# Kernel optimization log

Hardware: AMD Instinct MI355X
Metric: run time of the kernel (lower is better)

## Reference

```python
import jax, jax.numpy as jnp
import numpy as np
import math

B, S, N_EMBD, HEAD_SIZE = 32, 2048, 64, 64

def setup_inputs() -> dict:
    key = jax.random.key(0)
    k1, k2, k3, k4 = jax.random.split(key, 4)
    inputs = jax.random.normal(k1, (B, S, N_EMBD), dtype=jnp.float32)
    # nn.Linear(n_embd, head_size, bias=False) weights: shape (head_size, n_embd)
    scale = 1.0 / math.sqrt(N_EMBD)
    Wq = jax.random.normal(k2, (HEAD_SIZE, N_EMBD), dtype=jnp.float32) * scale
    Wk = jax.random.normal(k3, (HEAD_SIZE, N_EMBD), dtype=jnp.float32) * scale
    Wv = jax.random.normal(k4, (HEAD_SIZE, N_EMBD), dtype=jnp.float32) * scale
    return {"inputs": inputs, "Wq": Wq, "Wk": Wk, "Wv": Wv}

def reference(inputs, Wq, Wk, Wv):
    # q, k, v: [B, S, head_size]
    q = jnp.einsum('bse,he->bsh', inputs, Wq)
    k = jnp.einsum('bse,he->bsh', inputs, Wk)
    v = jnp.einsum('bse,he->bsh', inputs, Wv)
    scores = jnp.einsum('bqh,bkh->bqk', q, k) / jnp.sqrt(jnp.float32(HEAD_SIZE))
    # NOTE: the original torch code calls scores.masked_fill(...) out-of-place
    # and discards the result, so NO causal mask is actually applied.
    attention = jax.nn.softmax(scores, axis=-1)
    out = jnp.einsum('bqk,bkh->bqh', attention, v)  # [B, S, head_size]
    return out
```

## Files before the change

### kernel.cpp

```cpp
#include <hip/hip_runtime.h>


#define BATCH 32
#define SEQ   2048
#define HS    64
#define QSCALE 0.18033688011112042f
#define OTS   72
#define MSTR  68

typedef _Float16 f16x8 __attribute__((ext_vector_type(8)));
typedef _Float16 f16x4 __attribute__((ext_vector_type(4)));
typedef float    f32x4 __attribute__((ext_vector_type(4)));
typedef unsigned int u32x4 __attribute__((ext_vector_type(4)));

__global__ __launch_bounds__(256) void proj_kernel(
    const float* __restrict__ x, const float* __restrict__ Wq,
    const float* __restrict__ Wk, const float* __restrict__ Wv,
    _Float16* __restrict__ Qh, _Float16* __restrict__ Kh,
    _Float16* __restrict__ Vt)
{
    __shared__ __align__(16) _Float16 Wl[3 * 4096];
    __shared__ __align__(16) _Float16 ot[64 * OTS];

    const int t    = threadIdx.x;
    const int w    = t >> 6;
    const int lane = t & 63;
    const int lo   = lane & 15;
    const int quad = lane >> 4;

    {
#pragma unroll
        for (int c = 0; c < 6; ++c) {
            int id  = c * 256 + t;
            int m   = id >> 9;
            int rem = id & 511;
            int row = rem >> 3;
            int q8  = rem & 7;
            const float* Ws = (m == 0) ? Wq : ((m == 1) ? Wk : Wv);
            const float* sp = Ws + row * 64 + q8 * 8;
            float4 a0 = *(const float4*)sp;
            float4 a1 = *(const float4*)(sp + 4);
            float sc = (m == 0) ? QSCALE : 1.0f;
            f16x8 h;
            h[0]=(_Float16)(a0.x*sc); h[1]=(_Float16)(a0.y*sc);
            h[2]=(_Float16)(a0.z*sc); h[3]=(_Float16)(a0.w*sc);
            h[4]=(_Float16)(a1.x*sc); h[5]=(_Float16)(a1.y*sc);
            h[6]=(_Float16)(a1.z*sc); h[7]=(_Float16)(a1.w*sc);
            *(f16x8*)(Wl + m * 4096 + row * 64 + ((q8 ^ (row & 7)) << 3)) = h;
        }
    }

    const long blk0 = (long)blockIdx.x * 64;
    const int  b    = (int)(blk0 / SEQ);
    const int  s0   = (int)(blk0 % SEQ);
    const long rw   = blk0 + w * 16;

    const float* xp = x + (rw + lo) * HS + quad * 8;
    float4 x0 = *(const float4*)xp;
    float4 x1 = *(const float4*)(xp + 4);
    float4 x2 = *(const float4*)(xp + 32);
    float4 x3 = *(const float4*)(xp + 36);
    f16x8 xb0, xb1;
    xb0[0]=(_Float16)x0.x; xb0[1]=(_Float16)x0.y; xb0[2]=(_Float16)x0.z; xb0[3]=(_Float16)x0.w;
    xb0[4]=(_Float16)x1.x; xb0[5]=(_Float16)x1.y; xb0[6]=(_Float16)x1.z; xb0[7]=(_Float16)x1.w;
    xb1[0]=(_Float16)x2.x; xb1[1]=(_Float16)x2.y; xb1[2]=(_Float16)x2.z; xb1[3]=(_Float16)x2.w;
    xb1[4]=(_Float16)x3.x; xb1[5]=(_Float16)x3.y; xb1[6]=(_Float16)x3.z; xb1[7]=(_Float16)x3.w;

    __syncthreads();

#pragma unroll
    for (int m = 0; m < 3; ++m) {
        const _Float16* Wm = Wl + m * 4096;
        f32x4 acc[4];
#pragma unroll
        for (int nt = 0; nt < 4; ++nt) { acc[nt][0]=0.f; acc[nt][1]=0.f; acc[nt][2]=0.f; acc[nt][3]=0.f; }
#pragma unroll
        for (int nt = 0; nt < 4; ++nt) {
            f16x8 wa0 = *(const f16x8*)(Wm + (nt * 16 + lo) * 64 + (((quad    ) ^ (lo & 7)) << 3));
            f16x8 wa1 = *(const f16x8*)(Wm + (nt * 16 + lo) * 64 + (((4 + quad) ^ (lo & 7)) << 3));
            acc[nt] = __builtin_amdgcn_mfma_f32_16x16x32_f16(wa0, xb0, acc[nt], 0, 0, 0);
            acc[nt] = __builtin_amdgcn_mfma_f32_16x16x32_f16(wa1, xb1, acc[nt], 0, 0, 0);
        }
        if (m < 2) {
            _Float16* dst = (m == 0) ? Qh : Kh;
#pragma unroll
            for (int nt = 0; nt < 4; ++nt) {
                f16x4 pk;
                pk[0]=(_Float16)acc[nt][0]; pk[1]=(_Float16)acc[nt][1];
                pk[2]=(_Float16)acc[nt][2]; pk[3]=(_Float16)acc[nt][3];
                *(f16x4*)(dst + (rw + lo) * HS + nt * 16 + quad * 4) = pk;
            }
        } else {
#pragma unroll
            for (int nt = 0; nt < 4; ++nt)
#pragma unroll
                for (int r = 0; r < 4; ++r)
                    ot[(nt * 16 + quad * 4 + r) * OTS + w * 16 + lo] = (_Float16)acc[nt][r];
            __syncthreads();
            const int row = t >> 2, c = t & 3;
            f16x8 r0 = *(const f16x8*)(ot + row * OTS + c * 16);
            f16x8 r1 = *(const f16x8*)(ot + row * OTS + c * 16 + 8);
            _Float16* vd = Vt + ((long)b * HS + row) * SEQ + s0 + c * 16;
            *(f16x8*)vd       = r0;
            *(f16x8*)(vd + 8) = r1;
        }
    }
}

__global__ __launch_bounds__(256, 2) void attn_kernel(
    const _Float16* __restrict__ Q, const _Float16* __restrict__ K,
    const _Float16* __restrict__ Vt, float* __restrict__ out)
{
    __shared__ __align__(16) char smem[65536];
    _Float16* KVb  = (_Float16*)smem;
    float*    obuf = (float*)smem;
    float*    lbuf = obuf + 128 * MSTR;

    const int t    = threadIdx.x;
    const int w    = t >> 6;
    const int lane = t & 63;
    const int lo   = lane & 15;
    const int quad = lane >> 4;
    const int sr   = t >> 2, sc = t & 3;
    const int xr   = lo & 7;

    const int bid = blockIdx.x;
    const int b   = (bid & 7) | ((bid >> 7) << 3);
    const int qt  = (bid >> 3) & 15;
    const int q0  = qt * 128;
    const int qh  = w >> 1;
    const int kh  = w & 1;

    const _Float16* Qb = Q + ((long)b * SEQ + q0 + qh * 64) * HS;
    f16x8 qf[4][2];
#pragma unroll
    for (int q2 = 0; q2 < 4; ++q2) {
        qf[q2][0] = *(const f16x8*)(Qb + (q2 * 16 + lo) * HS + quad * 8);
        qf[q2][1] = *(const f16x8*)(Qb + (q2 * 16 + lo) * HS + 32 + quad * 8);
    }

    const _Float16* Kb = K  + (long)b * SEQ * HS;
    const _Float16* Vb = Vt + (long)b * HS * SEQ;

    const int pr  = (sr & 32) | ((sr & 4) << 2) | ((sr & 24) >> 1) | (sr & 3);
    const int kw0 = pr * 64 + (((2 * sc    ) ^ (pr & 7)) << 3);
    const int kw1 = pr * 64 + (((2 * sc + 1) ^ (pr & 7)) << 3);
    const int vw0 = 4096 + sr * 64 + (((2 * sc    ) ^ (sr & 7)) << 3);
    const int vw1 = 4096 + sr * 64 + (((2 * sc + 1) ^ (sr & 7)) << 3);

    const int kr0 = (kh * 32      + lo) * 64;
    const int kr1 = (kh * 32 + 16 + lo) * 64;
    const int g0  = ((quad    ) ^ xr) << 3;
    const int g1  = ((4 + quad) ^ xr) << 3;
    int voff[4];
#pragma unroll
    for (int ht = 0; ht < 4; ++ht)
        voff[ht] = 4096 + (ht * 16 + lo) * 64 + (((kh * 4 + quad) ^ xr) << 3);

    f32x4 o[4][4], ol[4];
#pragma unroll
    for (int q2 = 0; q2 < 4; ++q2) {
        ol[q2][0]=0.f; ol[q2][1]=0.f; ol[q2][2]=0.f; ol[q2][3]=0.f;
#pragma unroll
        for (int ht = 0; ht < 4; ++ht) { o[q2][ht][0]=0.f; o[q2][ht][1]=0.f; o[q2][ht][2]=0.f; o[q2][ht][3]=0.f; }
    }
    f32x4 zz; zz[0]=0.f; zz[1]=0.f; zz[2]=0.f; zz[3]=0.f;
    f16x8 ones;
#pragma unroll
    for (int j = 0; j < 8; ++j) ones[j] = (_Float16)1.0f;

    const int phase = qt << 1;
    const int key0 = (phase & 31) << 6;
    f16x8 kfA0 = *(const f16x8*)(Kb + (long)(key0 + sr) * HS + sc * 16);
    f16x8 kfB0 = *(const f16x8*)(Kb + (long)(key0 + sr) * HS + sc * 16 + 8);
    f16x8 vfA0 = *(const f16x8*)(Vb + (long)sr * SEQ + key0 + sc * 16);
    f16x8 vfB0 = *(const f16x8*)(Vb + (long)sr * SEQ + key0 + sc * 16 + 8);
    f16x8 kfA1 = *(const f16x8*)(Kb + (long)(key0 + 64 + sr) * HS + sc * 16);
    f16x8 kfB1 = *(const f16x8*)(Kb + (long)(key0 + 64 + sr) * HS + sc * 16 + 8);
    f16x8 vfA1 = *(const f16x8*)(Vb + (long)sr * SEQ + key0 + 64 + sc * 16);
    f16x8 vfB1 = *(const f16x8*)(Vb + (long)sr * SEQ + key0 + 64 + sc * 16 + 8);

    for (int kt2 = 0; kt2 < 16; ++kt2) {
        _Float16* Bp = KVb + (kt2 & 1) * 16384;
        *(f16x8*)(Bp + kw0) = kfA0;
        *(f16x8*)(Bp + kw1) = kfB0;
        *(f16x8*)(Bp + vw0) = vfA0;
        *(f16x8*)(Bp + vw1) = vfB0;
        *(f16x8*)(Bp + 8192 + kw0) = kfA1;
        *(f16x8*)(Bp + 8192 + kw1) = kfB1;
        *(f16x8*)(Bp + 8192 + vw0) = vfA1;
        *(f16x8*)(Bp + 8192 + vw1) = vfB1;

        const int keyn = ((2 * kt2 + 2 + phase) & 31) << 6;
        kfA0 = *(const f16x8*)(Kb + (long)(keyn + sr) * HS + sc * 16);
        kfB0 = *(const f16x8*)(Kb + (long)(keyn + sr) * HS + sc * 16 + 8);
        vfA0 = *(const f16x8*)(Vb + (long)sr * SEQ + keyn + sc * 16);
        vfB0 = *(const f16x8*)(Vb + (long)sr * SEQ + keyn + sc * 16 + 8);
        kfA1 = *(const f16x8*)(Kb + (long)(keyn + 64 + sr) * HS + sc * 16);
        kfB1 = *(const f16x8*)(Kb + (long)(keyn + 64 + sr) * HS + sc * 16 + 8);
        vfA1 = *(const f16x8*)(Vb + (long)sr * SEQ + keyn + 64 + sc * 16);
        vfB1 = *(const f16x8*)(Vb + (long)sr * SEQ + keyn + 64 + sc * 16 + 8);

        __syncthreads();

#pragma unroll
        for (int sub = 0; sub < 2; ++sub) {
            _Float16* Ksp = Bp + sub * 8192;

            f16x8 ka00 = *(const f16x8*)(Ksp + kr0 + g0);
            f16x8 ka01 = *(const f16x8*)(Ksp + kr0 + g1);
            f16x8 ka10 = *(const f16x8*)(Ksp + kr1 + g0);
            f16x8 ka11 = *(const f16x8*)(Ksp + kr1 + g1);

            f16x8 vbf[4];
#pragma unroll
            for (int ht = 0; ht < 4; ++ht)
                vbf[ht] = *(const f16x8*)(Ksp + voff[ht]);

#pragma unroll
            for (int q2 = 0; q2 < 4; ++q2) {
                f32x4 s0, s1;
                s0 = __builtin_amdgcn_mfma_f32_16x16x32_f16(ka00, qf[q2][0], zz, 0, 0, 0);
                s0 = __builtin_amdgcn_mfma_f32_16x16x32_f16(ka01, qf[q2][1], s0, 0, 0, 0);
                s1 = __builtin_amdgcn_mfma_f32_16x16x32_f16(ka10, qf[q2][0], zz, 0, 0, 0);
                s1 = __builtin_amdgcn_mfma_f32_16x16x32_f16(ka11, qf[q2][1], s1, 0, 0, 0);

                u32x4 pw;
                pw[0] = __builtin_bit_cast(unsigned int,
                        __builtin_amdgcn_cvt_pkrtz(__builtin_amdgcn_exp2f(s0[0]),
                                                   __builtin_amdgcn_exp2f(s0[1])));
                pw[1] = __builtin_bit_cast(unsigned int,
                        __builtin_amdgcn_cvt_pkrtz(__builtin_amdgcn_exp2f(s0[2]),
                                                   __builtin_amdgcn_exp2f(s0[3])));
                pw[2] = __builtin_bit_cast(unsigned int,
                        __builtin_amdgcn_cvt_pkrtz(__builtin_amdgcn_exp2f(s1[0]),
                                                   __builtin_amdgcn_exp2f(s1[1])));
                pw[3] = __builtin_bit_cast(unsigned int,
                        __builtin_amdgcn_cvt_pkrtz(__builtin_amdgcn_exp2f(s1[2]),
                                                   __builtin_amdgcn_exp2f(s1[3])));
                f16x8 pa = __builtin_bit_cast(f16x8, pw);

                ol[q2] = __builtin_amdgcn_mfma_f32_16x16x32_f16(pa, ones, ol[q2], 0, 0, 0);
#pragma unroll
                for (int ht = 0; ht < 4; ++ht)
                    o[q2][ht] = __builtin_amdgcn_mfma_f32_16x16x32_f16(pa, vbf[ht], o[q2][ht], 0, 0, 0);
            }
        }
    }

    __syncthreads();
    if (kh == 0) {
#pragma unroll
        for (int q2 = 0; q2 < 4; ++q2) {
#pragma unroll
            for (int ht = 0; ht < 4; ++ht)
#pragma unroll
                for (int r = 0; r < 4; ++r)
                    obuf[(qh * 64 + q2 * 16 + quad * 4 + r) * MSTR + ht * 16 + lo] = o[q2][ht][r];
            if (lo == 0) {
#pragma unroll
                for (int r = 0; r < 4; ++r)
                    lbuf[qh * 64 + q2 * 16 + quad * 4 + r] = ol[q2][r];
            }
        }
    }
    __syncthreads();
    if (kh == 1) {
#pragma unroll
        for (int q2 = 0; q2 < 4; ++q2) {
            float linv[4];
#pragma unroll
            for (int r = 0; r < 4; ++r)
                linv[r] = 1.0f / (lbuf[qh * 64 + q2 * 16 + quad * 4 + r] + ol[q2][r]);
#pragma unroll
            for (int ht = 0; ht < 4; ++ht)
#pragma unroll
                for (int r = 0; r < 4; ++r) {
                    const int row = qh * 64 + q2 * 16 + quad * 4 + r;
                    float v = (obuf[row * MSTR + ht * 16 + lo] + o[q2][ht][r]) * linv[r];
                    out[((long)b * SEQ + q0 + row) * HS + ht * 16 + lo] = v;
                }
        }
    }
}

extern "C" void kernel_launch(void* const* d_in, const int* in_sizes, int n_in,
                              void* d_out, int out_size, void* d_ws, size_t ws_size,
                              hipStream_t stream)
{
    const float* x  = (const float*)d_in[0];
    const float* Wq = (const float*)d_in[1];
    const float* Wk = (const float*)d_in[2];
    const float* Wv = (const float*)d_in[3];
    float* out = (float*)d_out;

    const size_t E = (size_t)BATCH * SEQ * HS;
    _Float16* Qh = (_Float16*)d_ws;
    _Float16* Kh = Qh + E;
    _Float16* Vt = Kh + E;

    proj_kernel<<<(BATCH * SEQ) / 64, 256, 0, stream>>>(x, Wq, Wk, Wv, Qh, Kh, Vt);
    attn_kernel<<<BATCH * (SEQ / 128), 256, 0, stream>>>(Qh, Kh, Vt, out);
}
```

Measured before the change: 118.4 us.

## Load K/V fragments directly from global memory, removing LDS staging and barriers

```diff
diff --git a/kernel.cpp b/kernel.cpp
--- a/kernel.cpp
+++ b/kernel.cpp
@@ -111,18 +111,14 @@
     const _Float16* __restrict__ Q, const _Float16* __restrict__ K,
     const _Float16* __restrict__ Vt, float* __restrict__ out)
 {
-    __shared__ __align__(16) char smem[65536];
-    _Float16* KVb  = (_Float16*)smem;
-    float*    obuf = (float*)smem;
-    float*    lbuf = obuf + 128 * MSTR;
+    __shared__ __align__(16) float obuf[128 * MSTR];
+    __shared__ __align__(16) float lbuf[128];
 
     const int t    = threadIdx.x;
     const int w    = t >> 6;
     const int lane = t & 63;
     const int lo   = lane & 15;
     const int quad = lane >> 4;
-    const int sr   = t >> 2, sc = t & 3;
-    const int xr   = lo & 7;
 
     const int bid = blockIdx.x;
     const int b   = (bid & 7) | ((bid >> 7) << 3);
@@ -142,20 +138,14 @@
     const _Float16* Kb = K  + (long)b * SEQ * HS;
     const _Float16* Vb = Vt + (long)b * HS * SEQ;
 
-    const int pr  = (sr & 32) | ((sr & 4) << 2) | ((sr & 24) >> 1) | (sr & 3);
-    const int kw0 = pr * 64 + (((2 * sc    ) ^ (pr & 7)) << 3);
-    const int kw1 = pr * 64 + (((2 * sc + 1) ^ (pr & 7)) << 3);
-    const int vw0 = 4096 + sr * 64 + (((2 * sc    ) ^ (sr & 7)) << 3);
-    const int vw1 = 4096 + sr * 64 + (((2 * sc + 1) ^ (sr & 7)) << 3);
-
-    const int kr0 = (kh * 32      + lo) * 64;
-    const int kr1 = (kh * 32 + 16 + lo) * 64;
-    const int g0  = ((quad    ) ^ xr) << 3;
-    const int g1  = ((4 + quad) ^ xr) << 3;
-    int voff[4];
-#pragma unroll
-    for (int ht = 0; ht < 4; ++ht)
-        voff[ht] = 4096 + (ht * 16 + lo) * 64 + (((kh * 4 + quad) ^ xr) << 3);
+    const int p0  = kh * 32 + lo;
+    const int p1  = kh * 32 + 16 + lo;
+    const int k00 = (p0 & 0x23) | ((p0 & 8) << 1) | ((p0 & 4) << 1) | ((p0 & 16) >> 2);
+    const int k10 = (p1 & 0x23) | ((p1 & 8) << 1) | ((p1 & 4) << 1) | ((p1 & 16) >> 2);
+
+    const _Float16* kp0 = Kb + k00 * 64 + quad * 8;
+    const _Float16* kp1 = Kb + k10 * 64 + quad * 8;
+    const _Float16* vp  = Vb + kh * 32 + quad * 8;
 
     f32x4 o[4][4], ol[4];
 #pragma unroll
@@ -169,86 +159,52 @@
 #pragma unroll
     for (int j = 0; j < 8; ++j) ones[j] = (_Float16)1.0f;
 
-    const int phase = qt << 1;
-    const int key0 = (phase & 31) << 6;
-    f16x8 kfA0 = *(const f16x8*)(Kb + (long)(key0 + sr) * HS + sc * 16);
-    f16x8 kfB0 = *(const f16x8*)(Kb + (long)(key0 + sr) * HS + sc * 16 + 8);
-    f16x8 vfA0 = *(const f16x8*)(Vb + (long)sr * SEQ + key0 + sc * 16);
-    f16x8 vfB0 = *(const f16x8*)(Vb + (long)sr * SEQ + key0 + sc * 16 + 8);
-    f16x8 kfA1 = *(const f16x8*)(Kb + (long)(key0 + 64 + sr) * HS + sc * 16);
-    f16x8 kfB1 = *(const f16x8*)(Kb + (long)(key0 + 64 + sr) * HS + sc * 16 + 8);
-    f16x8 vfA1 = *(const f16x8*)(Vb + (long)sr * SEQ + key0 + 64 + sc * 16);
-    f16x8 vfB1 = *(const f16x8*)(Vb + (long)sr * SEQ + key0 + 64 + sc * 16 + 8);
-
-    for (int kt2 = 0; kt2 < 16; ++kt2) {
-        _Float16* Bp = KVb + (kt2 & 1) * 16384;
-        *(f16x8*)(Bp + kw0) = kfA0;
-        *(f16x8*)(Bp + kw1) = kfB0;
-        *(f16x8*)(Bp + vw0) = vfA0;
-        *(f16x8*)(Bp + vw1) = vfB0;
-        *(f16x8*)(Bp + 8192 + kw0) = kfA1;
-        *(f16x8*)(Bp + 8192 + kw1) = kfB1;
-        *(f16x8*)(Bp + 8192 + vw0) = vfA1;
-        *(f16x8*)(Bp + 8192 + vw1) = vfB1;
-
-        const int keyn = ((2 * kt2 + 2 + phase) & 31) << 6;
-        kfA0 = *(const f16x8*)(Kb + (long)(keyn + sr) * HS + sc * 16);
-        kfB0 = *(const f16x8*)(Kb + (long)(keyn + sr) * HS + sc * 16 + 8);
-        vfA0 = *(const f16x8*)(Vb + (long)sr * SEQ + keyn + sc * 16);
-        vfB0 = *(const f16x8*)(Vb + (long)sr * SEQ + keyn + sc * 16 + 8);
-        kfA1 = *(const f16x8*)(Kb + (long)(keyn + 64 + sr) * HS + sc * 16);
-        kfB1 = *(const f16x8*)(Kb + (long)(keyn + 64 + sr) * HS + sc * 16 + 8);
-        vfA1 = *(const f16x8*)(Vb + (long)sr * SEQ + keyn + 64 + sc * 16);
-        vfB1 = *(const f16x8*)(Vb + (long)sr * SEQ + keyn + 64 + sc * 16 + 8);
-
-        __syncthreads();
-
-#pragma unroll
-        for (int sub = 0; sub < 2; ++sub) {
-            _Float16* Ksp = Bp + sub * 8192;
-
-            f16x8 ka00 = *(const f16x8*)(Ksp + kr0 + g0);
-            f16x8 ka01 = *(const f16x8*)(Ksp + kr0 + g1);
-            f16x8 ka10 = *(const f16x8*)(Ksp + kr1 + g0);
-            f16x8 ka11 = *(const f16x8*)(Ksp + kr1 + g1);
-
-            f16x8 vbf[4];
+    const int phase = (qt << 1) & 31;
+
+#pragma unroll 2
+    for (int kt = 0; kt < 32; ++kt) {
+        const int keyA = ((kt + phase) & 31) << 6;
+
+        f16x8 ka00 = *(const f16x8*)(kp0 + keyA * 64);
+        f16x8 ka01 = *(const f16x8*)(kp0 + keyA * 64 + 32);
+        f16x8 ka10 = *(const f16x8*)(kp1 + keyA * 64);
+        f16x8 ka11 = *(const f16x8*)(kp1 + keyA * 64 + 32);
+
+        f16x8 vbf[4];
+#pragma unroll
+        for (int ht = 0; ht < 4; ++ht)
+            vbf[ht] = *(const f16x8*)(vp + (ht * 16 + lo) * SEQ + keyA);
+
+#pragma unroll
+        for (int q2 = 0; q2 < 4; ++q2) {
+            f32x4 s0, s1;
+            s0 = __builtin_amdgcn_mfma_f32_16x16x32_f16(ka00, qf[q2][0], zz, 0, 0, 0);
+            s0 = __builtin_amdgcn_mfma_f32_16x16x32_f16(ka01, qf[q2][1], s0, 0, 0, 0);
+            s1 = __builtin_amdgcn_mfma_f32_16x16x32_f16(ka10, qf[q2][0], zz, 0, 0, 0);
+            s1 = __builtin_amdgcn_mfma_f32_16x16x32_f16(ka11, qf[q2][1], s1, 0, 0, 0);
+
+            u32x4 pw;
+            pw[0] = __builtin_bit_cast(unsigned int,
+                    __builtin_amdgcn_cvt_pkrtz(__builtin_amdgcn_exp2f(s0[0]),
+                                               __builtin_amdgcn_exp2f(s0[1])));
+            pw[1] = __builtin_bit_cast(unsigned int,
+                    __builtin_amdgcn_cvt_pkrtz(__builtin_amdgcn_exp2f(s0[2]),
+                                               __builtin_amdgcn_exp2f(s0[3])));
+            pw[2] = __builtin_bit_cast(unsigned int,
+                    __builtin_amdgcn_cvt_pkrtz(__builtin_amdgcn_exp2f(s1[0]),
+                                               __builtin_amdgcn_exp2f(s1[1])));
+            pw[3] = __builtin_bit_cast(unsigned int,
+                    __builtin_amdgcn_cvt_pkrtz(__builtin_amdgcn_exp2f(s1[2]),
+                                               __builtin_amdgcn_exp2f(s1[3])));
+            f16x8 pa = __builtin_bit_cast(f16x8, pw);
+
+            ol[q2] = __builtin_amdgcn_mfma_f32_16x16x32_f16(pa, ones, ol[q2], 0, 0, 0);
 #pragma unroll
             for (int ht = 0; ht < 4; ++ht)
-                vbf[ht] = *(const f16x8*)(Ksp + voff[ht]);
-
-#pragma unroll
-            for (int q2 = 0; q2 < 4; ++q2) {
-                f32x4 s0, s1;
-                s0 = __builtin_amdgcn_mfma_f32_16x16x32_f16(ka00, qf[q2][0], zz, 0, 0, 0);
-                s0 = __builtin_amdgcn_mfma_f32_16x16x32_f16(ka01, qf[q2][1], s0, 0, 0, 0);
-                s1 = __builtin_amdgcn_mfma_f32_16x16x32_f16(ka10, qf[q2][0], zz, 0, 0, 0);
-                s1 = __builtin_amdgcn_mfma_f32_16x16x32_f16(ka11, qf[q2][1], s1, 0, 0, 0);
-
-                u32x4 pw;
-                pw[0] = __builtin_bit_cast(unsigned int,
-                        __builtin_amdgcn_cvt_pkrtz(__builtin_amdgcn_exp2f(s0[0]),
-                                                   __builtin_amdgcn_exp2f(s0[1])));
-                pw[1] = __builtin_bit_cast(unsigned int,
-                        __builtin_amdgcn_cvt_pkrtz(__builtin_amdgcn_exp2f(s0[2]),
-                                                   __builtin_amdgcn_exp2f(s0[3])));
-                pw[2] = __builtin_bit_cast(unsigned int,
-                        __builtin_amdgcn_cvt_pkrtz(__builtin_amdgcn_exp2f(s1[0]),
-                                                   __builtin_amdgcn_exp2f(s1[1])));
-                pw[3] = __builtin_bit_cast(unsigned int,
-                        __builtin_amdgcn_cvt_pkrtz(__builtin_amdgcn_exp2f(s1[2]),
-                                                   __builtin_amdgcn_exp2f(s1[3])));
-                f16x8 pa = __builtin_bit_cast(f16x8, pw);
-
-                ol[q2] = __builtin_amdgcn_mfma_f32_16x16x32_f16(pa, ones, ol[q2], 0, 0, 0);
-#pragma unroll
-                for (int ht = 0; ht < 4; ++ht)
-                    o[q2][ht] = __builtin_amdgcn_mfma_f32_16x16x32_f16(pa, vbf[ht], o[q2][ht], 0, 0, 0);
-            }
-        }
-    }
-
-    __syncthreads();
+                o[q2][ht] = __builtin_amdgcn_mfma_f32_16x16x32_f16(pa, vbf[ht], o[q2][ht], 0, 0, 0);
+        }
+    }
+
     if (kh == 0) {
 #pragma unroll
         for (int q2 = 0; q2 < 4; ++q2) {
```

Result: slower. 143.9 us (+21.6%).

## Halve attention query tile to 64 rows and stage single 64-key tiles

Applied to the files above, without the earlier changes.

```diff
diff --git a/kernel.cpp b/kernel.cpp
--- a/kernel.cpp
+++ b/kernel.cpp
@@ -107,14 +107,14 @@
     }
 }
 
-__global__ __launch_bounds__(256, 2) void attn_kernel(
+__global__ __launch_bounds__(256) void attn_kernel(
     const _Float16* __restrict__ Q, const _Float16* __restrict__ K,
     const _Float16* __restrict__ Vt, float* __restrict__ out)
 {
-    __shared__ __align__(16) char smem[65536];
+    __shared__ __align__(16) char smem[32768];
     _Float16* KVb  = (_Float16*)smem;
     float*    obuf = (float*)smem;
-    float*    lbuf = obuf + 128 * MSTR;
+    float*    lbuf = obuf + 64 * MSTR;
 
     const int t    = threadIdx.x;
     const int w    = t >> 6;
@@ -125,16 +125,16 @@
     const int xr   = lo & 7;
 
     const int bid = blockIdx.x;
-    const int b   = (bid & 7) | ((bid >> 7) << 3);
-    const int qt  = (bid >> 3) & 15;
-    const int q0  = qt * 128;
+    const int b   = (bid & 7) | ((bid >> 8) << 3);
+    const int qt  = (bid >> 3) & 31;
+    const int q0  = qt * 64;
     const int qh  = w >> 1;
     const int kh  = w & 1;
 
-    const _Float16* Qb = Q + ((long)b * SEQ + q0 + qh * 64) * HS;
-    f16x8 qf[4][2];
-#pragma unroll
-    for (int q2 = 0; q2 < 4; ++q2) {
+    const _Float16* Qb = Q + ((long)b * SEQ + q0 + qh * 32) * HS;
+    f16x8 qf[2][2];
+#pragma unroll
+    for (int q2 = 0; q2 < 2; ++q2) {
         qf[q2][0] = *(const f16x8*)(Qb + (q2 * 16 + lo) * HS + quad * 8);
         qf[q2][1] = *(const f16x8*)(Qb + (q2 * 16 + lo) * HS + 32 + quad * 8);
     }
@@ -157,9 +157,9 @@
     for (int ht = 0; ht < 4; ++ht)
         voff[ht] = 4096 + (ht * 16 + lo) * 64 + (((kh * 4 + quad) ^ xr) << 3);
 
-    f32x4 o[4][4], ol[4];
-#pragma unroll
-    for (int q2 = 0; q2 < 4; ++q2) {
+    f32x4 o[2][4], ol[2];
+#pragma unroll
+    for (int q2 = 0; q2 < 2; ++q2) {
         ol[q2][0]=0.f; ol[q2][1]=0.f; ol[q2][2]=0.f; ol[q2][3]=0.f;
 #pragma unroll
         for (int ht = 0; ht < 4; ++ht) { o[q2][ht][0]=0.f; o[q2][ht][1]=0.f; o[q2][ht][2]=0.f; o[q2][ht][3]=0.f; }
@@ -169,114 +169,97 @@
 #pragma unroll
     for (int j = 0; j < 8; ++j) ones[j] = (_Float16)1.0f;
 
-    const int phase = qt << 1;
-    const int key0 = (phase & 31) << 6;
-    f16x8 kfA0 = *(const f16x8*)(Kb + (long)(key0 + sr) * HS + sc * 16);
-    f16x8 kfB0 = *(const f16x8*)(Kb + (long)(key0 + sr) * HS + sc * 16 + 8);
-    f16x8 vfA0 = *(const f16x8*)(Vb + (long)sr * SEQ + key0 + sc * 16);
-    f16x8 vfB0 = *(const f16x8*)(Vb + (long)sr * SEQ + key0 + sc * 16 + 8);
-    f16x8 kfA1 = *(const f16x8*)(Kb + (long)(key0 + 64 + sr) * HS + sc * 16);
-    f16x8 kfB1 = *(const f16x8*)(Kb + (long)(key0 + 64 + sr) * HS + sc * 16 + 8);
-    f16x8 vfA1 = *(const f16x8*)(Vb + (long)sr * SEQ + key0 + 64 + sc * 16);
-    f16x8 vfB1 = *(const f16x8*)(Vb + (long)sr * SEQ + key0 + 64 + sc * 16 + 8);
-
-    for (int kt2 = 0; kt2 < 16; ++kt2) {
-        _Float16* Bp = KVb + (kt2 & 1) * 16384;
-        *(f16x8*)(Bp + kw0) = kfA0;
-        *(f16x8*)(Bp + kw1) = kfB0;
-        *(f16x8*)(Bp + vw0) = vfA0;
-        *(f16x8*)(Bp + vw1) = vfB0;
-        *(f16x8*)(Bp + 8192 + kw0) = kfA1;
-        *(f16x8*)(Bp + 8192 + kw1) = kfB1;
-        *(f16x8*)(Bp + 8192 + vw0) = vfA1;
-        *(f16x8*)(Bp + 8192 + vw1) = vfB1;
-
-        const int keyn = ((2 * kt2 + 2 + phase) & 31) << 6;
-        kfA0 = *(const f16x8*)(Kb + (long)(keyn + sr) * HS + sc * 16);
-        kfB0 = *(const f16x8*)(Kb + (long)(keyn + sr) * HS + sc * 16 + 8);
-        vfA0 = *(const f16x8*)(Vb + (long)sr * SEQ + keyn + sc * 16);
-        vfB0 = *(const f16x8*)(Vb + (long)sr * SEQ + keyn + sc * 16 + 8);
-        kfA1 = *(const f16x8*)(Kb + (long)(keyn + 64 + sr) * HS + sc * 16);
-        kfB1 = *(const f16x8*)(Kb + (long)(keyn + 64 + sr) * HS + sc * 16 + 8);
-        vfA1 = *(const f16x8*)(Vb + (long)sr * SEQ + keyn + 64 + sc * 16);
-        vfB1 = *(const f16x8*)(Vb + (long)sr * SEQ + keyn + 64 + sc * 16 + 8);
+    const int phase = qt & 31;
+    const int key0  = phase << 6;
+    f16x8 kfA = *(const f16x8*)(Kb + (long)(key0 + sr) * HS + sc * 16);
+    f16x8 kfB = *(const f16x8*)(Kb + (long)(key0 + sr) * HS + sc * 16 + 8);
+    f16x8 vfA = *(const f16x8*)(Vb + (long)sr * SEQ + key0 + sc * 16);
+    f16x8 vfB = *(const f16x8*)(Vb + (long)sr * SEQ + key0 + sc * 16 + 8);
+
+    for (int kt = 0; kt < 32; ++kt) {
+        _Float16* Ksp = KVb + (kt & 1) * 8192;
+        *(f16x8*)(Ksp + kw0) = kfA;
+        *(f16x8*)(Ksp + kw1) = kfB;
+        *(f16x8*)(Ksp + vw0) = vfA;
+        *(f16x8*)(Ksp + vw1) = vfB;
+
+        const int keyn = ((kt + 1 + phase) & 31) << 6;
+        kfA = *(const f16x8*)(Kb + (long)(keyn + sr) * HS + sc * 16);
+        kfB = *(const f16x8*)(Kb + (long)(keyn + sr) * HS + sc * 16 + 8);
+        vfA = *(const f16x8*)(Vb + (long)sr * SEQ + keyn + sc * 16);
+        vfB = *(const f16x8*)(Vb + (long)sr * SEQ + keyn + sc * 16 + 8);
 
         __syncthreads();
 
-#pragma unroll
-        for (int sub = 0; sub < 2; ++sub) {
-            _Float16* Ksp = Bp + sub * 8192;
-
-            f16x8 ka00 = *(const f16x8*)(Ksp + kr0 + g0);
-            f16x8 ka01 = *(const f16x8*)(Ksp + kr0 + g1);
-            f16x8 ka10 = *(const f16x8*)(Ksp + kr1 + g0);
-            f16x8 ka11 = *(const f16x8*)(Ksp + kr1 + g1);
-
-            f16x8 vbf[4];
+        f16x8 ka00 = *(const f16x8*)(Ksp + kr0 + g0);
+        f16x8 ka01 = *(const f16x8*)(Ksp + kr0 + g1);
+        f16x8 ka10 = *(const f16x8*)(Ksp + kr1 + g0);
+        f16x8 ka11 = *(const f16x8*)(Ksp + kr1 + g1);
+
+        f16x8 vbf[4];
+#pragma unroll
+        for (int ht = 0; ht < 4; ++ht)
+            vbf[ht] = *(const f16x8*)(Ksp + voff[ht]);
+
+#pragma unroll
+        for (int q2 = 0; q2 < 2; ++q2) {
+            f32x4 s0, s1;
+            s0 = __builtin_amdgcn_mfma_f32_16x16x32_f16(ka00, qf[q2][0], zz, 0, 0, 0);
+            s0 = __builtin_amdgcn_mfma_f32_16x16x32_f16(ka01, qf[q2][1], s0, 0, 0, 0);
+            s1 = __builtin_amdgcn_mfma_f32_16x16x32_f16(ka10, qf[q2][0], zz, 0, 0, 0);
+            s1 = __builtin_amdgcn_mfma_f32_16x16x32_f16(ka11, qf[q2][1], s1, 0, 0, 0);
+
+            u32x4 pw;
+            pw[0] = __builtin_bit_cast(unsigned int,
+                    __builtin_amdgcn_cvt_pkrtz(__builtin_amdgcn_exp2f(s0[0]),
+                                               __builtin_amdgcn_exp2f(s0[1])));
+            pw[1] = __builtin_bit_cast(unsigned int,
+                    __builtin_amdgcn_cvt_pkrtz(__builtin_amdgcn_exp2f(s0[2]),
+                                               __builtin_amdgcn_exp2f(s0[3])));
+            pw[2] = __builtin_bit_cast(unsigned int,
+                    __builtin_amdgcn_cvt_pkrtz(__builtin_amdgcn_exp2f(s1[0]),
+                                               __builtin_amdgcn_exp2f(s1[1])));
+            pw[3] = __builtin_bit_cast(unsigned int,
+                    __builtin_amdgcn_cvt_pkrtz(__builtin_amdgcn_exp2f(s1[2]),
+                                               __builtin_amdgcn_exp2f(s1[3])));
+            f16x8 pa = __builtin_bit_cast(f16x8, pw);
+
+            ol[q2] = __builtin_amdgcn_mfma_f32_16x16x32_f16(pa, ones, ol[q2], 0, 0, 0);
 #pragma unroll
             for (int ht = 0; ht < 4; ++ht)
-                vbf[ht] = *(const f16x8*)(Ksp + voff[ht]);
-
-#pragma unroll
-            for (int q2 = 0; q2 < 4; ++q2) {
-                f32x4 s0, s1;
-                s0 = __builtin_amdgcn_mfma_f32_16x16x32_f16(ka00, qf[q2][0], zz, 0, 0, 0);
-                s0 = __builtin_amdgcn_mfma_f32_16x16x32_f16(ka01, qf[q2][1], s0, 0, 0, 0);
-                s1 = __builtin_amdgcn_mfma_f32_16x16x32_f16(ka10, qf[q2][0], zz, 0, 0, 0);
-                s1 = __builtin_amdgcn_mfma_f32_16x16x32_f16(ka11, qf[q2][1], s1, 0, 0, 0);
-
-                u32x4 pw;
-                pw[0] = __builtin_bit_cast(unsigned int,
-                        __builtin_amdgcn_cvt_pkrtz(__builtin_amdgcn_exp2f(s0[0]),
-                                                   __builtin_amdgcn_exp2f(s0[1])));
-                pw[1] = __builtin_bit_cast(unsigned int,
-                        __builtin_amdgcn_cvt_pkrtz(__builtin_amdgcn_exp2f(s0[2]),
-                                                   __builtin_amdgcn_exp2f(s0[3])));
-                pw[2] = __builtin_bit_cast(unsigned int,
-                        __builtin_amdgcn_cvt_pkrtz(__builtin_amdgcn_exp2f(s1[0]),
-                                                   __builtin_amdgcn_exp2f(s1[1])));
-                pw[3] = __builtin_bit_cast(unsigned int,
-                        __builtin_amdgcn_cvt_pkrtz(__builtin_amdgcn_exp2f(s1[2]),
-                                                   __builtin_amdgcn_exp2f(s1[3])));
-                f16x8 pa = __builtin_bit_cast(f16x8, pw);
-
-                ol[q2] = __builtin_amdgcn_mfma_f32_16x16x32_f16(pa, ones, ol[q2], 0, 0, 0);
-#pragma unroll
-                for (int ht = 0; ht < 4; ++ht)
-                    o[q2][ht] = __builtin_amdgcn_mfma_f32_16x16x32_f16(pa, vbf[ht], o[q2][ht], 0, 0, 0);
-            }
+                o[q2][ht] = __builtin_amdgcn_mfma_f32_16x16x32_f16(pa, vbf[ht], o[q2][ht], 0, 0, 0);
         }
     }
 
     __syncthreads();
     if (kh == 0) {
 #pragma unroll
-        for (int q2 = 0; q2 < 4; ++q2) {
+        for (int q2 = 0; q2 < 2; ++q2) {
 #pragma unroll
             for (int ht = 0; ht < 4; ++ht)
 #pragma unroll
                 for (int r = 0; r < 4; ++r)
-                    obuf[(qh * 64 + q2 * 16 + quad * 4 + r) * MSTR + ht * 16 + lo] = o[q2][ht][r];
+                    obuf[(qh * 32 + q2 * 16 + quad * 4 + r) * MSTR + ht * 16 + lo] = o[q2][ht][r];
             if (lo == 0) {
 #pragma unroll
                 for (int r = 0; r < 4; ++r)
-                    lbuf[qh * 64 + q2 * 16 + quad * 4 + r] = ol[q2][r];
+                    lbuf[qh * 32 + q2 * 16 + quad * 4 + r] = ol[q2][r];
             }
         }
     }
     __syncthreads();
     if (kh == 1) {
 #pragma unroll
-        for (int q2 = 0; q2 < 4; ++q2) {
+        for (int q2 = 0; q2 < 2; ++q2) {
             float linv[4];
 #pragma unroll
             for (int r = 0; r < 4; ++r)
-                linv[r] = 1.0f / (lbuf[qh * 64 + q2 * 16 + quad * 4 + r] + ol[q2][r]);
+                linv[r] = 1.0f / (lbuf[qh * 32 + q2 * 16 + quad * 4 + r] + ol[q2][r]);
 #pragma unroll
             for (int ht = 0; ht < 4; ++ht)
 #pragma unroll
                 for (int r = 0; r < 4; ++r) {
-                    const int row = qh * 64 + q2 * 16 + quad * 4 + r;
+                    const int row = qh * 32 + q2 * 16 + quad * 4 + r;
                     float v = (obuf[row * MSTR + ht * 16 + lo] + o[q2][ht][r]) * linv[r];
                     out[((long)b * SEQ + q0 + row) * HS + ht * 16 + lo] = v;
                 }
@@ -300,5 +283,5 @@
     _Float16* Vt = Kh + E;
 
     proj_kernel<<<(BATCH * SEQ) / 64, 256, 0, stream>>>(x, Wq, Wk, Wv, Qh, Kh, Vt);
-    attn_kernel<<<BATCH * (SEQ / 128), 256, 0, stream>>>(Qh, Kh, Vt, out);
+    attn_kernel<<<BATCH * (SEQ / 64), 256, 0, stream>>>(Qh, Kh, Vt, out);
 }
```

Measured after the change: 135.2 us. 14.3% more time.
